# Optimization experiments

Measured on AMD Instinct MI355X. Metric: run time of the kernel, lower is better.

The kernel has to match this reference:

```python
import jax, jax.numpy as jnp
import numpy as np

DIM = 256
HEADS = 8
DK = DIM // HEADS
MLP_HID = 4 * DIM
EPS = 1e-5


def _ln(t, s, b):
    m = jnp.mean(t, axis=-1, keepdims=True)
    v = jnp.mean((t - m) ** 2, axis=-1, keepdims=True)
    return (t - m) / jnp.sqrt(v + EPS) * s + b


def setup_inputs() -> dict:
    key = jax.random.key(0)
    ks = jax.random.split(key, 32)
    B, N, C = 8, 128, DIM
    d = {}
    d["x"] = jax.random.normal(ks[0], (B, N, C), jnp.float32)
    d["y"] = jax.random.normal(ks[1], (B, N, N, C), jnp.float32)
    def lin(k, fi, fo):
        k1, k2 = jax.random.split(k)
        return (jax.random.normal(k1, (fi, fo), jnp.float32) * 0.02,
                jax.random.normal(k2, (fo,), jnp.float32) * 0.02)
    for i, nm in enumerate(["q", "k", "v", "e", "oe", "on"]):
        w, b = lin(ks[2 + i], C, C)
        d[f"W{nm}"], d[f"b{nm}"] = w, b
    for i, nm in enumerate(["mlp1", "mlp2"]):
        w1, b1 = lin(ks[10 + 2 * i], C, MLP_HID)
        w2, b2 = lin(ks[11 + 2 * i], MLP_HID, C)
        d[f"{nm}_w1"], d[f"{nm}_b1"] = w1, b1
        d[f"{nm}_w2"], d[f"{nm}_b2"] = w2, b2
    for i, nm in enumerate(["ln1", "ln3", "ln4", "ln5", "ln6"]):
        d[f"{nm}_s"] = jnp.ones((C,), jnp.float32)
        d[f"{nm}_b"] = jnp.zeros((C,), jnp.float32)
    return d


def reference(x, y, Wq, bq, Wk, bk, Wv, bv, We, be, Woe, boe, Won, bon,
              mlp1_w1, mlp1_b1, mlp1_w2, mlp1_b2,
              mlp2_w1, mlp2_b1, mlp2_w2, mlp2_b2,
              ln1_s, ln1_b, ln3_s, ln3_b, ln4_s, ln4_b,
              ln5_s, ln5_b, ln6_s, ln6_b):
    B, N, C = x.shape
    H, DKl = HEADS, DK

    x1 = _ln(x, ln1_s, ln1_b)

    # attention (elementwise q*k modulated by edge embeddings)
    q = (x1 @ Wq + bq).reshape(B, N, H, DKl)
    k = (x1 @ Wk + bk).reshape(B, N, H, DKl)
    v = (x1 @ Wv + bv).reshape(B, N, H, DKl)
    e = (y @ We + be).reshape(B, N, N, H, DKl)

    attn = q[:, :, None] * k[:, None, :]          # (B,N,N,H,DK)
    attn = attn / jnp.sqrt(jnp.float32(DKl))
    attn = attn * (e + 1.0) * e

    edge_out = attn.reshape(B, N, N, C) @ Woe + boe  # out_e
    p = jax.nn.softmax(attn, axis=2)                 # softmax over second n
    agg = jnp.einsum("bijhd,bjhd->bihd", p, v).reshape(B, N, C)
    node_out = agg @ Won + bon                       # out_n

    x2 = _ln(x1 + node_out, ln3_s, ln3_b)
    y2 = _ln(edge_out + y, ln4_s, ln4_b)

    mlp_x = jax.nn.relu(x2 @ mlp1_w1 + mlp1_b1) @ mlp1_w2 + mlp1_b2
    mlp_y = jax.nn.relu(y2 @ mlp2_w1 + mlp2_b1) @ mlp2_w2 + mlp2_b2

    x_out = _ln(x2 + mlp_x, ln5_s, ln5_b)
    y_out = _ln(y2 + mlp_y, ln6_s, ln6_b)
    return (x_out, y_out)
```

## Files before the change

kernel.cpp:

```cpp
#include <hip/hip_runtime.h>

#define CDIM 256
#define NSEQ 128
#define HID 1024
#define EPS 1e-5f
#define SCALE 0.17677669529663687f
#define ASTR 264
#define MROWS 64

typedef __attribute__((ext_vector_type(8))) short short8;
typedef __attribute__((ext_vector_type(4))) float f32x4;

static __device__ __forceinline__ unsigned short f2bf(float x) {
    unsigned u = __float_as_uint(x);
    u += 0x7fff + ((u >> 16) & 1);
    return (unsigned short)(u >> 16);
}
static __device__ __forceinline__ float bf2f(unsigned short h) {
    return __uint_as_float(((unsigned)h) << 16);
}

__global__ __launch_bounds__(256) void prep_w(const float* __restrict__ W,
        unsigned short* __restrict__ hi, unsigned short* __restrict__ lo,
        int N, int ksBits) {
    int idx = blockIdx.x * 256 + threadIdx.x;
    int j = idx & 7, lane = (idx >> 3) & 63, rest = idx >> 9;
    int ks = rest & ((1 << ksBits) - 1), nt = rest >> ksBits;
    int n = nt * 16 + (lane & 15);
    int kk = ks * 32 + ((lane >> 4) << 3) + j;
    float x = W[kk * N + n];
    unsigned short h = f2bf(x);
    hi[idx] = h;
    lo[idx] = f2bf(x - bf2f(h));
}

__device__ __forceinline__ float2 block_ln(float val, float* sred) {
    const int wave = threadIdx.x >> 6;
    const int lane = threadIdx.x & 63;
    float s = val, ss = val * val;
    #pragma unroll
    for (int off = 32; off; off >>= 1) {
        s  += __shfl_xor(s, off);
        ss += __shfl_xor(ss, off);
    }
    __syncthreads();
    if (lane == 0) { sred[wave] = s; sred[4 + wave] = ss; }
    __syncthreads();
    s  = sred[0] + sred[1] + sred[2] + sred[3];
    ss = sred[4] + sred[5] + sred[6] + sred[7];
    float mu = s * (1.f / 256.f);
    float rs = rsqrtf(ss * (1.f / 256.f) - mu * mu + EPS);
    return make_float2(mu, rs);
}

__global__ __launch_bounds__(256) void ln1_kernel(
    const float* __restrict__ x, const float* __restrict__ s,
    const float* __restrict__ b, float* __restrict__ x1) {
    __shared__ float sred[8];
    const int bi = blockIdx.x, t = threadIdx.x;
    float v = x[bi * CDIM + t];
    float2 mr = block_ln(v, sred);
    x1[bi * CDIM + t] = (v - mr.x) * mr.y * s[t] + b[t];
}

__global__ __launch_bounds__(256) void qkv_kernel(
    const float* __restrict__ x1,
    const float* __restrict__ Wq, const float* __restrict__ bq,
    const float* __restrict__ Wk, const float* __restrict__ bk,
    const float* __restrict__ Wv, const float* __restrict__ bv,
    float* __restrict__ q, float* __restrict__ k, float* __restrict__ v) {
    __shared__ float sX[CDIM];
    const int bi = blockIdx.x, t = threadIdx.x;
    sX[t] = x1[bi * CDIM + t];
    __syncthreads();
    float aq = bq[t], ak = bk[t], av = bv[t];
    for (int kk = 0; kk < CDIM; kk += 4) {
        float4 xv = *(const float4*)&sX[kk];
        #pragma unroll
        for (int d = 0; d < 4; ++d) {
            float xd = (d == 0) ? xv.x : (d == 1) ? xv.y : (d == 2) ? xv.z : xv.w;
            aq += xd * Wq[(kk + d) * CDIM + t];
            ak += xd * Wk[(kk + d) * CDIM + t];
            av += xd * Wv[(kk + d) * CDIM + t];
        }
    }
    q[bi * CDIM + t] = aq;
    k[bi * CDIM + t] = ak;
    v[bi * CDIM + t] = av;
}

static __device__ __forceinline__ void gemm16(
    const unsigned short* __restrict__ Ah, const unsigned short* __restrict__ Al,
    const unsigned short* __restrict__ Bh, const unsigned short* __restrict__ Bl,
    int nt0, int ksTotal, int ks0, int lane, f32x4 acc[4][2])
{
    const int l16 = lane & 15, quad = lane >> 4;
    #pragma unroll 2
    for (int ks = 0; ks < 8; ++ks) {
        short8 bh[2], bl[2];
        #pragma unroll
        for (int nt = 0; nt < 2; ++nt) {
            size_t off = ((size_t)((nt0 + nt) * ksTotal + (ks0 + ks)) * 64 + lane) * 8;
            bh[nt] = *(const short8*)(Bh + off);
            bl[nt] = *(const short8*)(Bl + off);
        }
        #pragma unroll
        for (int mt = 0; mt < 4; ++mt) {
            int ao = (mt * 16 + l16) * ASTR + ks * 32 + quad * 8;
            short8 ah = *(const short8*)(Ah + ao);
            short8 al = *(const short8*)(Al + ao);
            #pragma unroll
            for (int nt = 0; nt < 2; ++nt) {
                acc[mt][nt] = __builtin_amdgcn_mfma_f32_16x16x32_bf16(ah, bh[nt], acc[mt][nt], 0, 0, 0);
                acc[mt][nt] = __builtin_amdgcn_mfma_f32_16x16x32_bf16(ah, bl[nt], acc[mt][nt], 0, 0, 0);
                acc[mt][nt] = __builtin_amdgcn_mfma_f32_16x16x32_bf16(al, bh[nt], acc[mt][nt], 0, 0, 0);
            }
        }
    }
}

static __device__ __forceinline__ void ln_reduce(
    float pre[4][2][4], float* sSum, float* sSS, int w, int l16, int quad, int tid)
{
    #pragma unroll
    for (int mt = 0; mt < 4; ++mt)
        #pragma unroll
        for (int r = 0; r < 4; ++r) {
            float s  = pre[mt][0][r] + pre[mt][1][r];
            float ss = pre[mt][0][r] * pre[mt][0][r] + pre[mt][1][r] * pre[mt][1][r];
            #pragma unroll
            for (int off = 1; off < 16; off <<= 1) {
                s  += __shfl_xor(s, off);
                ss += __shfl_xor(ss, off);
            }
            if (l16 == 0) {
                int row = mt * 16 + quad * 4 + r;
                sSum[w * 64 + row] = s;
                sSS [w * 64 + row] = ss;
            }
        }
    __syncthreads();
    if (tid < 64) {
        float S = 0.f, SS2 = 0.f;
        #pragma unroll
        for (int ww = 0; ww < 8; ++ww) { S += sSum[ww * 64 + tid]; SS2 += sSS[ww * 64 + tid]; }
        float mu = S * (1.f / 256.f);
        float rs = rsqrtf(SS2 * (1.f / 256.f) - mu * mu + EPS);
        sSum[tid] = mu; sSS[tid] = rs;
    }
    __syncthreads();
}

__global__ __launch_bounds__(512, 2) void y_mega(
    const float* __restrict__ y, const float* __restrict__ qg, const float* __restrict__ kg,
    const unsigned short* __restrict__ WeH, const unsigned short* __restrict__ WeL,
    const float* __restrict__ be,
    const unsigned short* __restrict__ WoH, const unsigned short* __restrict__ WoL,
    const float* __restrict__ boe,
    const unsigned short* __restrict__ W1H, const unsigned short* __restrict__ W1L,
    const float* __restrict__ b1,
    const unsigned short* __restrict__ W2H, const unsigned short* __restrict__ W2L,
    const float* __restrict__ b2,
    const float* __restrict__ ln4s, const float* __restrict__ ln4b,
    const float* __restrict__ ln6s, const float* __restrict__ ln6b,
    unsigned short* __restrict__ attn_bf, float* __restrict__ yout)
{
    __shared__ unsigned short sAh[MROWS * ASTR], sAl[MROWS * ASTR];
    __shared__ unsigned short sHh[MROWS * ASTR], sHl[MROWS * ASTR];
    __shared__ float sSum[8 * 64], sSS[8 * 64];

    const int tid  = threadIdx.x;
    const int w    = tid >> 6, lane = tid & 63;
    const int l16  = lane & 15, quad = lane >> 4;
    const long long row0 = (long long)blockIdx.x * MROWS;
    const int b  = (int)(row0 >> 14);
    const int i  = (int)((row0 >> 7) & 127);
    const int j0 = (int)(row0 & 127);
    const float* qrow  = qg + ((b << 7) + i) * CDIM;
    const float* kbase = kg + ((b << 7) + j0) * CDIM;
    const int c0 = w * 32 + l16, c1 = c0 + 16;

    {
        int r  = tid >> 3;
        int cc = (tid & 7) * 32;
        const float* src = y + (row0 + r) * CDIM + cc;
        unsigned short hbuf[32], lbuf[32];
        #pragma unroll
        for (int e = 0; e < 32; e += 4) {
            float4 vv = *(const float4*)(src + e);
            float a[4] = {vv.x, vv.y, vv.z, vv.w};
            #pragma unroll
            for (int d = 0; d < 4; ++d) {
                unsigned short h = f2bf(a[d]);
                hbuf[e + d] = h;
                lbuf[e + d] = f2bf(a[d] - bf2f(h));
            }
        }
        #pragma unroll
        for (int e = 0; e < 32; e += 8) {
            *(short8*)&sAh[r * ASTR + cc + e] = *(short8*)&hbuf[e];
            *(short8*)&sAl[r * ASTR + cc + e] = *(short8*)&lbuf[e];
        }
    }
    __syncthreads();

    f32x4 acc[4][2];
    const f32x4 zf = {0.f, 0.f, 0.f, 0.f};

    #pragma unroll
    for (int mt = 0; mt < 4; ++mt) { acc[mt][0] = zf; acc[mt][1] = zf; }
    gemm16(sAh, sAl, WeH, WeL, w * 2, 8, 0, lane, acc);

    float q0 = qrow[c0], q1 = qrow[c1];
    float be0 = be[c0], be1 = be[c1];
    float attnv[4][2][4];
    #pragma unroll
    for (int mt = 0; mt < 4; ++mt)
        #pragma unroll
        for (int r = 0; r < 4; ++r) {
            int mloc = mt * 16 + quad * 4 + r;
            float k0 = kbase[mloc * CDIM + c0], k1 = kbase[mloc * CDIM + c1];
            float e0 = acc[mt][0][r] + be0, e1 = acc[mt][1][r] + be1;
            float a0 = q0 * k0 * SCALE * ((e0 + 1.f) * e0);
            float a1 = q1 * k1 * SCALE * ((e1 + 1.f) * e1);
            attnv[mt][0][r] = a0; attnv[mt][1][r] = a1;
            attn_bf[(row0 + mloc) * CDIM + c0] = f2bf(a0);
            attn_bf[(row0 + mloc) * CDIM + c1] = f2bf(a1);
        }
    __syncthreads();

    #pragma unroll
    for (int mt = 0; mt < 4; ++mt)
        #pragma unroll
        for (int r = 0; r < 4; ++r) {
            int mloc = mt * 16 + quad * 4 + r;
            #pragma unroll
            for (int nt = 0; nt < 2; ++nt) {
                int c = (nt == 0) ? c0 : c1;
                float a = attnv[mt][nt][r];
                unsigned short h = f2bf(a);
                sAh[mloc * ASTR + c] = h;
                sAl[mloc * ASTR + c] = f2bf(a - bf2f(h));
            }
        }
    __syncthreads();

    #pragma unroll
    for (int mt = 0; mt < 4; ++mt) { acc[mt][0] = zf; acc[mt][1] = zf; }
    gemm16(sAh, sAl, WoH, WoL, w * 2, 8, 0, lane, acc);

    float pre[4][2][4];
    float bo0 = boe[c0], bo1 = boe[c1];
    #pragma unroll
    for (int mt = 0; mt < 4; ++mt)
        #pragma unroll
        for (int r = 0; r < 4; ++r) {
            int mloc = mt * 16 + quad * 4 + r;
            pre[mt][0][r] = acc[mt][0][r] + bo0 + y[(row0 + mloc) * CDIM + c0];
            pre[mt][1][r] = acc[mt][1][r] + bo1 + y[(row0 + mloc) * CDIM + c1];
        }
    ln_reduce(pre, sSum, sSS, w, l16, quad, tid);

    float l4s0 = ln4s[c0], l4b0 = ln4b[c0], l4s1 = ln4s[c1], l4b1 = ln4b[c1];
    float y2v[4][2][4];
    #pragma unroll
    for (int mt = 0; mt < 4; ++mt)
        #pragma unroll
        for (int r = 0; r < 4; ++r) {
            int mloc = mt * 16 + quad * 4 + r;
            float mu = sSum[mloc], rs = sSS[mloc];
            float v0 = (pre[mt][0][r] - mu) * rs * l4s0 + l4b0;
            float v1 = (pre[mt][1][r] - mu) * rs * l4s1 + l4b1;
            y2v[mt][0][r] = v0; y2v[mt][1][r] = v1;
            unsigned short h0 = f2bf(v0), h1 = f2bf(v1);
            sAh[mloc * ASTR + c0] = h0; sAl[mloc * ASTR + c0] = f2bf(v0 - bf2f(h0));
            sAh[mloc * ASTR + c1] = h1; sAl[mloc * ASTR + c1] = f2bf(v1 - bf2f(h1));
        }
    __syncthreads();

    f32x4 out[4][2];
    #pragma unroll
    for (int mt = 0; mt < 4; ++mt) { out[mt][0] = zf; out[mt][1] = zf; }
    for (int qq = 0; qq < 4; ++qq) {
        f32x4 hh[4][2];
        #pragma unroll
        for (int mt = 0; mt < 4; ++mt) { hh[mt][0] = zf; hh[mt][1] = zf; }
        gemm16(sAh, sAl, W1H, W1L, qq * 16 + w * 2, 8, 0, lane, hh);
        float bb0 = b1[qq * 256 + c0], bb1 = b1[qq * 256 + c1];
        __syncthreads();
        #pragma unroll
        for (int mt = 0; mt < 4; ++mt)
            #pragma unroll
            for (int r = 0; r < 4; ++r) {
                int mloc = mt * 16 + quad * 4 + r;
                float h0 = fmaxf(hh[mt][0][r] + bb0, 0.f);
                float h1 = fmaxf(hh[mt][1][r] + bb1, 0.f);
                unsigned short hb0 = f2bf(h0), hb1 = f2bf(h1);
                sHh[mloc * ASTR + c0] = hb0; sHl[mloc * ASTR + c0] = f2bf(h0 - bf2f(hb0));
                sHh[mloc * ASTR + c1] = hb1; sHl[mloc * ASTR + c1] = f2bf(h1 - bf2f(hb1));
            }
        __syncthreads();
        gemm16(sHh, sHl, W2H, W2L, w * 2, 32, qq * 8, lane, out);
    }

    float b20 = b2[c0], b21 = b2[c1];
    #pragma unroll
    for (int mt = 0; mt < 4; ++mt)
        #pragma unroll
        for (int r = 0; r < 4; ++r) {
            pre[mt][0][r] = y2v[mt][0][r] + out[mt][0][r] + b20;
            pre[mt][1][r] = y2v[mt][1][r] + out[mt][1][r] + b21;
        }
    __syncthreads();
    ln_reduce(pre, sSum, sSS, w, l16, quad, tid);

    float l6s0 = ln6s[c0], l6b0 = ln6b[c0], l6s1 = ln6s[c1], l6b1 = ln6b[c1];
    #pragma unroll
    for (int mt = 0; mt < 4; ++mt)
        #pragma unroll
        for (int r = 0; r < 4; ++r) {
            int mloc = mt * 16 + quad * 4 + r;
            float mu = sSum[mloc], rs = sSS[mloc];
            yout[(row0 + mloc) * CDIM + c0] = (pre[mt][0][r] - mu) * rs * l6s0 + l6b0;
            yout[(row0 + mloc) * CDIM + c1] = (pre[mt][1][r] - mu) * rs * l6s1 + l6b1;
        }
}

__global__ __launch_bounds__(256) void softmax_agg(
    const unsigned short* __restrict__ attn, const float* __restrict__ v,
    float* __restrict__ agg) {
    const int bi = blockIdx.x, t = threadIdx.x;
    const unsigned short* ap = attn + (long long)bi * NSEQ * CDIM + t;
    const float* vp = v + (long long)(bi >> 7) * NSEQ * CDIM + t;
    float m = -1e30f;
    for (int j = 0; j < NSEQ; ++j) m = fmaxf(m, bf2f(ap[j * CDIM]));
    float s = 0.f, o = 0.f;
    for (int j = 0; j < NSEQ; ++j) {
        float ex = __expf(bf2f(ap[j * CDIM]) - m);
        s += ex;
        o += ex * vp[j * CDIM];
    }
    agg[bi * CDIM + t] = o / s;
}

__global__ __launch_bounds__(256) void x_path(
    const float* __restrict__ x1, const float* __restrict__ agg,
    const float* __restrict__ Won, const float* __restrict__ bon,
    const float* __restrict__ ln3s, const float* __restrict__ ln3b,
    const float* __restrict__ w1, const float* __restrict__ b1,
    const float* __restrict__ w2, const float* __restrict__ b2,
    const float* __restrict__ ln5s, const float* __restrict__ ln5b,
    float* __restrict__ xout) {
    __shared__ float sG[CDIM];
    __shared__ float sX2[CDIM];
    __shared__ float sH[HID];
    __shared__ float sred[8];
    const int bi = blockIdx.x, t = threadIdx.x;
    sG[t] = agg[bi * CDIM + t];
    __syncthreads();
    float no = bon[t];
    for (int kk = 0; kk < CDIM; kk += 4) {
        float4 gv = *(const float4*)&sG[kk];
        no += gv.x * Won[(kk + 0) * CDIM + t] + gv.y * Won[(kk + 1) * CDIM + t]
            + gv.z * Won[(kk + 2) * CDIM + t] + gv.w * Won[(kk + 3) * CDIM + t];
    }
    float pre = x1[bi * CDIM + t] + no;
    float2 mr = block_ln(pre, sred);
    float x2 = (pre - mr.x) * mr.y * ln3s[t] + ln3b[t];
    sX2[t] = x2;
    __syncthreads();
    float h[4];
    #pragma unroll
    for (int m = 0; m < 4; ++m) h[m] = b1[t + 256 * m];
    for (int kk = 0; kk < CDIM; kk += 4) {
        float4 xv = *(const float4*)&sX2[kk];
        #pragma unroll
        for (int m = 0; m < 4; ++m) {
            int u = t + 256 * m;
            h[m] += xv.x * w1[(kk + 0) * HID + u] + xv.y * w1[(kk + 1) * HID + u]
                  + xv.z * w1[(kk + 2) * HID + u] + xv.w * w1[(kk + 3) * HID + u];
        }
    }
    #pragma unroll
    for (int m = 0; m < 4; ++m) sH[t + 256 * m] = fmaxf(h[m], 0.f);
    __syncthreads();
    float o = b2[t];
    for (int u = 0; u < HID; u += 4) {
        float4 hv = *(const float4*)&sH[u];
        o += hv.x * w2[(u + 0) * CDIM + t] + hv.y * w2[(u + 1) * CDIM + t]
           + hv.z * w2[(u + 2) * CDIM + t] + hv.w * w2[(u + 3) * CDIM + t];
    }
    float pre2 = x2 + o;
    float2 mr2 = block_ln(pre2, sred);
    xout[bi * CDIM + t] = (pre2 - mr2.x) * mr2.y * ln5s[t] + ln5b[t];
}

extern "C" void kernel_launch(void* const* d_in, const int* in_sizes, int n_in,
                              void* d_out, int out_size, void* d_ws, size_t ws_size,
                              hipStream_t stream) {
    const float* x   = (const float*)d_in[0];
    const float* y   = (const float*)d_in[1];
    const float* Wq  = (const float*)d_in[2];  const float* bq  = (const float*)d_in[3];
    const float* Wk  = (const float*)d_in[4];  const float* bk  = (const float*)d_in[5];
    const float* Wv  = (const float*)d_in[6];  const float* bv  = (const float*)d_in[7];
    const float* We  = (const float*)d_in[8];  const float* be  = (const float*)d_in[9];
    const float* Woe = (const float*)d_in[10]; const float* boe = (const float*)d_in[11];
    const float* Won = (const float*)d_in[12]; const float* bon = (const float*)d_in[13];
    const float* m1w1= (const float*)d_in[14]; const float* m1b1= (const float*)d_in[15];
    const float* m1w2= (const float*)d_in[16]; const float* m1b2= (const float*)d_in[17];
    const float* m2w1= (const float*)d_in[18]; const float* m2b1= (const float*)d_in[19];
    const float* m2w2= (const float*)d_in[20]; const float* m2b2= (const float*)d_in[21];
    const float* ln1s= (const float*)d_in[22]; const float* ln1b= (const float*)d_in[23];
    const float* ln3s= (const float*)d_in[24]; const float* ln3b= (const float*)d_in[25];
    const float* ln4s= (const float*)d_in[26]; const float* ln4b= (const float*)d_in[27];
    const float* ln5s= (const float*)d_in[28]; const float* ln5b= (const float*)d_in[29];
    const float* ln6s= (const float*)d_in[30]; const float* ln6b= (const float*)d_in[31];

    const int BN  = 8 * 128;
    const long long BNN = 8LL * 128 * 128;

    float* ws  = (float*)d_ws;
    float* x1  = ws;
    float* q   = x1 + BN * CDIM;
    float* k   = q  + BN * CDIM;
    float* v   = k  + BN * CDIM;
    float* agg = v  + BN * CDIM;
    unsigned short* attn_bf = (unsigned short*)(agg + BN * CDIM);
    unsigned short* WeH = attn_bf + BNN * CDIM;
    unsigned short* WeL = WeH + 65536;
    unsigned short* WoH = WeL + 65536;
    unsigned short* WoL = WoH + 65536;
    unsigned short* W1H = WoL + 65536;
    unsigned short* W1L = W1H + 262144;
    unsigned short* W2H = W1L + 262144;
    unsigned short* W2L = W2H + 262144;

    float* xout = (float*)d_out;
    float* yout = xout + BN * CDIM;

    prep_w<<<256,  256, 0, stream>>>(We,   WeH, WeL, 256,  3);
    prep_w<<<256,  256, 0, stream>>>(Woe,  WoH, WoL, 256,  3);
    prep_w<<<1024, 256, 0, stream>>>(m2w1, W1H, W1L, 1024, 3);
    prep_w<<<1024, 256, 0, stream>>>(m2w2, W2H, W2L, 256,  5);

    ln1_kernel<<<BN, 256, 0, stream>>>(x, ln1s, ln1b, x1);
    qkv_kernel<<<BN, 256, 0, stream>>>(x1, Wq, bq, Wk, bk, Wv, bv, q, k, v);

    y_mega<<<(int)(BNN / MROWS), 512, 0, stream>>>(
        y, q, k, WeH, WeL, be, WoH, WoL, boe,
        W1H, W1L, m2b1, W2H, W2L, m2b2,
        ln4s, ln4b, ln6s, ln6b, attn_bf, yout);

    softmax_agg<<<BN, 256, 0, stream>>>(attn_bf, v, agg);
    x_path<<<BN, 256, 0, stream>>>(x1, agg, Won, bon, ln3s, ln3b,
                                   m1w1, m1b1, m1w2, m1b2, ln5s, ln5b, xout);
}
```

Measured before the change: 991.9 us.

## Shrink edge tile, drop low-bf16 weight terms, fuse prep and LN/QKV, batch node rows

The edge mega-kernel tile drops from 64 to 32 rows and the occupancy hint rises to 4 blocks per CU. The Woe, MLP1 and MLP2 GEMMs now use a two-term split-bf16 product instead of three, which skips the weight low-part MFMA and its loads at some cost in accuracy. The four weight-prep launches merge into one, and LN1 and QKV fuse into a single kernel that handles 4 rows per block. Softmax-aggregate splits j across two thread teams with paired-channel loads, and x_path processes 4 rows per block to reuse weight loads.

```diff
diff --git a/kernel.cpp b/kernel.cpp
--- a/kernel.cpp
+++ b/kernel.cpp
@@ -6,7 +6,7 @@
 #define EPS 1e-5f
 #define SCALE 0.17677669529663687f
 #define ASTR 264
-#define MROWS 64
+#define MROWS 32
 
 typedef __attribute__((ext_vector_type(8))) short short8;
 typedef __attribute__((ext_vector_type(4))) float f32x4;
@@ -20,79 +20,91 @@
     return __uint_as_float(((unsigned)h) << 16);
 }
 
-__global__ __launch_bounds__(256) void prep_w(const float* __restrict__ W,
-        unsigned short* __restrict__ hi, unsigned short* __restrict__ lo,
-        int N, int ksBits) {
-    int idx = blockIdx.x * 256 + threadIdx.x;
+__global__ __launch_bounds__(256) void prep_all(
+    const float* __restrict__ We, const float* __restrict__ Woe,
+    const float* __restrict__ W1, const float* __restrict__ W2,
+    unsigned short* __restrict__ WeH, unsigned short* __restrict__ WeL,
+    unsigned short* __restrict__ WoH, unsigned short* __restrict__ W1H,
+    unsigned short* __restrict__ W2H) {
+    int blk = blockIdx.x;
+    const float* W; unsigned short* H; unsigned short* L = nullptr;
+    int N, ksBits, base;
+    if (blk < 256)       { W = We;  H = WeH; L = WeL; N = 256;  ksBits = 3; base = 0; }
+    else if (blk < 512)  { W = Woe; H = WoH; N = 256;  ksBits = 3; base = 256; }
+    else if (blk < 1536) { W = W1;  H = W1H; N = 1024; ksBits = 3; base = 512; }
+    else                 { W = W2;  H = W2H; N = 256;  ksBits = 5; base = 1536; }
+    int idx = (blk - base) * 256 + threadIdx.x;
     int j = idx & 7, lane = (idx >> 3) & 63, rest = idx >> 9;
     int ks = rest & ((1 << ksBits) - 1), nt = rest >> ksBits;
-    int n = nt * 16 + (lane & 15);
+    int n  = nt * 16 + (lane & 15);
     int kk = ks * 32 + ((lane >> 4) << 3) + j;
     float x = W[kk * N + n];
     unsigned short h = f2bf(x);
-    hi[idx] = h;
-    lo[idx] = f2bf(x - bf2f(h));
-}
-
-__device__ __forceinline__ float2 block_ln(float val, float* sred) {
-    const int wave = threadIdx.x >> 6;
-    const int lane = threadIdx.x & 63;
-    float s = val, ss = val * val;
-    #pragma unroll
-    for (int off = 32; off; off >>= 1) {
-        s  += __shfl_xor(s, off);
-        ss += __shfl_xor(ss, off);
-    }
-    __syncthreads();
-    if (lane == 0) { sred[wave] = s; sred[4 + wave] = ss; }
-    __syncthreads();
-    s  = sred[0] + sred[1] + sred[2] + sred[3];
-    ss = sred[4] + sred[5] + sred[6] + sred[7];
-    float mu = s * (1.f / 256.f);
-    float rs = rsqrtf(ss * (1.f / 256.f) - mu * mu + EPS);
-    return make_float2(mu, rs);
-}
-
-__global__ __launch_bounds__(256) void ln1_kernel(
-    const float* __restrict__ x, const float* __restrict__ s,
-    const float* __restrict__ b, float* __restrict__ x1) {
-    __shared__ float sred[8];
-    const int bi = blockIdx.x, t = threadIdx.x;
-    float v = x[bi * CDIM + t];
-    float2 mr = block_ln(v, sred);
-    x1[bi * CDIM + t] = (v - mr.x) * mr.y * s[t] + b[t];
-}
-
-__global__ __launch_bounds__(256) void qkv_kernel(
-    const float* __restrict__ x1,
+    H[idx] = h;
+    if (L) L[idx] = f2bf(x - bf2f(h));
+}
+
+__global__ __launch_bounds__(256) void lnqkv_kernel(
+    const float* __restrict__ x,
+    const float* __restrict__ ln1s, const float* __restrict__ ln1b,
     const float* __restrict__ Wq, const float* __restrict__ bq,
     const float* __restrict__ Wk, const float* __restrict__ bk,
     const float* __restrict__ Wv, const float* __restrict__ bv,
+    float* __restrict__ x1,
     float* __restrict__ q, float* __restrict__ k, float* __restrict__ v) {
-    __shared__ float sX[CDIM];
-    const int bi = blockIdx.x, t = threadIdx.x;
-    sX[t] = x1[bi * CDIM + t];
-    __syncthreads();
-    float aq = bq[t], ak = bk[t], av = bv[t];
-    for (int kk = 0; kk < CDIM; kk += 4) {
-        float4 xv = *(const float4*)&sX[kk];
-        #pragma unroll
-        for (int d = 0; d < 4; ++d) {
-            float xd = (d == 0) ? xv.x : (d == 1) ? xv.y : (d == 2) ? xv.z : xv.w;
-            aq += xd * Wq[(kk + d) * CDIM + t];
-            ak += xd * Wk[(kk + d) * CDIM + t];
-            av += xd * Wv[(kk + d) * CDIM + t];
-        }
-    }
-    q[bi * CDIM + t] = aq;
-    k[bi * CDIM + t] = ak;
-    v[bi * CDIM + t] = av;
-}
-
-static __device__ __forceinline__ void gemm16(
-    const unsigned short* __restrict__ Ah, const unsigned short* __restrict__ Al,
+    __shared__ float sX[4][CDIM];
+    __shared__ float sMu[4], sRs[4];
+    const int bi0 = blockIdx.x * 4, t = threadIdx.x;
+    const int w = t >> 6, lane = t & 63;
+    float xv[4];
+    #pragma unroll
+    for (int r = 0; r < 4; ++r) { xv[r] = x[(bi0 + r) * CDIM + t]; sX[r][t] = xv[r]; }
+    __syncthreads();
+    {
+        float s = 0.f, ss = 0.f;
+        #pragma unroll
+        for (int m = 0; m < 4; ++m) { float a = sX[w][lane + 64 * m]; s += a; ss += a * a; }
+        #pragma unroll
+        for (int off = 32; off; off >>= 1) { s += __shfl_xor(s, off); ss += __shfl_xor(ss, off); }
+        if (lane == 0) {
+            float mu = s * (1.f / 256.f);
+            sMu[w] = mu;
+            sRs[w] = rsqrtf(ss * (1.f / 256.f) - mu * mu + EPS);
+        }
+    }
+    __syncthreads();
+    #pragma unroll
+    for (int r = 0; r < 4; ++r) {
+        float xn = (xv[r] - sMu[r]) * sRs[r] * ln1s[t] + ln1b[t];
+        sX[r][t] = xn;
+        x1[(bi0 + r) * CDIM + t] = xn;
+    }
+    __syncthreads();
+    float aq[4], ak[4], av[4];
+    #pragma unroll
+    for (int r = 0; r < 4; ++r) { aq[r] = bq[t]; ak[r] = bk[t]; av[r] = bv[t]; }
+    #pragma unroll 4
+    for (int kk = 0; kk < CDIM; ++kk) {
+        float wq = Wq[kk * CDIM + t], wk = Wk[kk * CDIM + t], wv = Wv[kk * CDIM + t];
+        #pragma unroll
+        for (int r = 0; r < 4; ++r) {
+            float xd = sX[r][kk];
+            aq[r] += xd * wq; ak[r] += xd * wk; av[r] += xd * wv;
+        }
+    }
+    #pragma unroll
+    for (int r = 0; r < 4; ++r) {
+        q[(bi0 + r) * CDIM + t] = aq[r];
+        k[(bi0 + r) * CDIM + t] = ak[r];
+        v[(bi0 + r) * CDIM + t] = av[r];
+    }
+}
+
+template <int TERMS>
+static __device__ __forceinline__ void gemmN(
+    const unsigned short* Ah, const unsigned short* Al,
     const unsigned short* __restrict__ Bh, const unsigned short* __restrict__ Bl,
-    int nt0, int ksTotal, int ks0, int lane, f32x4 acc[4][2])
+    int nt0, int ksTotal, int ks0, int lane, f32x4 acc[2][2])
 {
     const int l16 = lane & 15, quad = lane >> 4;
     #pragma unroll 2
@@ -102,28 +114,29 @@
         for (int nt = 0; nt < 2; ++nt) {
             size_t off = ((size_t)((nt0 + nt) * ksTotal + (ks0 + ks)) * 64 + lane) * 8;
             bh[nt] = *(const short8*)(Bh + off);
-            bl[nt] = *(const short8*)(Bl + off);
-        }
-        #pragma unroll
-        for (int mt = 0; mt < 4; ++mt) {
+            if (TERMS == 3) bl[nt] = *(const short8*)(Bl + off);
+        }
+        #pragma unroll
+        for (int mt = 0; mt < 2; ++mt) {
             int ao = (mt * 16 + l16) * ASTR + ks * 32 + quad * 8;
             short8 ah = *(const short8*)(Ah + ao);
             short8 al = *(const short8*)(Al + ao);
             #pragma unroll
             for (int nt = 0; nt < 2; ++nt) {
                 acc[mt][nt] = __builtin_amdgcn_mfma_f32_16x16x32_bf16(ah, bh[nt], acc[mt][nt], 0, 0, 0);
-                acc[mt][nt] = __builtin_amdgcn_mfma_f32_16x16x32_bf16(ah, bl[nt], acc[mt][nt], 0, 0, 0);
                 acc[mt][nt] = __builtin_amdgcn_mfma_f32_16x16x32_bf16(al, bh[nt], acc[mt][nt], 0, 0, 0);
+                if (TERMS == 3)
+                    acc[mt][nt] = __builtin_amdgcn_mfma_f32_16x16x32_bf16(ah, bl[nt], acc[mt][nt], 0, 0, 0);
             }
         }
     }
 }
 
-static __device__ __forceinline__ void ln_reduce(
-    float pre[4][2][4], float* sSum, float* sSS, int w, int l16, int quad, int tid)
+static __device__ __forceinline__ void ln_reduce32(
+    float pre[2][2][4], float* sSum, float* sSS, int w, int l16, int quad, int tid)
 {
     #pragma unroll
-    for (int mt = 0; mt < 4; ++mt)
+    for (int mt = 0; mt < 2; ++mt)
         #pragma unroll
         for (int r = 0; r < 4; ++r) {
             float s  = pre[mt][0][r] + pre[mt][1][r];
@@ -135,15 +148,15 @@
             }
             if (l16 == 0) {
                 int row = mt * 16 + quad * 4 + r;
-                sSum[w * 64 + row] = s;
-                sSS [w * 64 + row] = ss;
+                sSum[w * 32 + row] = s;
+                sSS [w * 32 + row] = ss;
             }
         }
     __syncthreads();
-    if (tid < 64) {
+    if (tid < 32) {
         float S = 0.f, SS2 = 0.f;
         #pragma unroll
-        for (int ww = 0; ww < 8; ++ww) { S += sSum[ww * 64 + tid]; SS2 += sSS[ww * 64 + tid]; }
+        for (int ww = 0; ww < 8; ++ww) { S += sSum[ww * 32 + tid]; SS2 += sSS[ww * 32 + tid]; }
         float mu = S * (1.f / 256.f);
         float rs = rsqrtf(SS2 * (1.f / 256.f) - mu * mu + EPS);
         sSum[tid] = mu; sSS[tid] = rs;
@@ -151,23 +164,20 @@
     __syncthreads();
 }
 
-__global__ __launch_bounds__(512, 2) void y_mega(
+__global__ __launch_bounds__(512, 4) void y_mega(
     const float* __restrict__ y, const float* __restrict__ qg, const float* __restrict__ kg,
     const unsigned short* __restrict__ WeH, const unsigned short* __restrict__ WeL,
     const float* __restrict__ be,
-    const unsigned short* __restrict__ WoH, const unsigned short* __restrict__ WoL,
-    const float* __restrict__ boe,
-    const unsigned short* __restrict__ W1H, const unsigned short* __restrict__ W1L,
-    const float* __restrict__ b1,
-    const unsigned short* __restrict__ W2H, const unsigned short* __restrict__ W2L,
-    const float* __restrict__ b2,
+    const unsigned short* __restrict__ WoH, const float* __restrict__ boe,
+    const unsigned short* __restrict__ W1H, const float* __restrict__ b1,
+    const unsigned short* __restrict__ W2H, const float* __restrict__ b2,
     const float* __restrict__ ln4s, const float* __restrict__ ln4b,
     const float* __restrict__ ln6s, const float* __restrict__ ln6b,
     unsigned short* __restrict__ attn_bf, float* __restrict__ yout)
 {
     __shared__ unsigned short sAh[MROWS * ASTR], sAl[MROWS * ASTR];
     __shared__ unsigned short sHh[MROWS * ASTR], sHl[MROWS * ASTR];
-    __shared__ float sSum[8 * 64], sSS[8 * 64];
+    __shared__ float sSum[8 * 32], sSS[8 * 32];
 
     const int tid  = threadIdx.x;
     const int w    = tid >> 6, lane = tid & 63;
@@ -181,12 +191,12 @@
     const int c0 = w * 32 + l16, c1 = c0 + 16;
 
     {
-        int r  = tid >> 3;
-        int cc = (tid & 7) * 32;
+        int r  = tid >> 4;
+        int cc = (tid & 15) * 16;
         const float* src = y + (row0 + r) * CDIM + cc;
-        unsigned short hbuf[32], lbuf[32];
-        #pragma unroll
-        for (int e = 0; e < 32; e += 4) {
+        unsigned short hbuf[16], lbuf[16];
+        #pragma unroll
+        for (int e = 0; e < 16; e += 4) {
             float4 vv = *(const float4*)(src + e);
             float a[4] = {vv.x, vv.y, vv.z, vv.w};
             #pragma unroll
@@ -197,25 +207,25 @@
             }
         }
         #pragma unroll
-        for (int e = 0; e < 32; e += 8) {
+        for (int e = 0; e < 16; e += 8) {
             *(short8*)&sAh[r * ASTR + cc + e] = *(short8*)&hbuf[e];
             *(short8*)&sAl[r * ASTR + cc + e] = *(short8*)&lbuf[e];
         }
     }
     __syncthreads();
 
-    f32x4 acc[4][2];
+    f32x4 acc[2][2];
     const f32x4 zf = {0.f, 0.f, 0.f, 0.f};
 
     #pragma unroll
-    for (int mt = 0; mt < 4; ++mt) { acc[mt][0] = zf; acc[mt][1] = zf; }
-    gemm16(sAh, sAl, WeH, WeL, w * 2, 8, 0, lane, acc);
+    for (int mt = 0; mt < 2; ++mt) { acc[mt][0] = zf; acc[mt][1] = zf; }
+    gemmN<3>(sAh, sAl, WeH, WeL, w * 2, 8, 0, lane, acc);
 
     float q0 = qrow[c0], q1 = qrow[c1];
     float be0 = be[c0], be1 = be[c1];
-    float attnv[4][2][4];
-    #pragma unroll
-    for (int mt = 0; mt < 4; ++mt)
+    float attnv[2][2][4];
+    #pragma unroll
+    for (int mt = 0; mt < 2; ++mt)
         #pragma unroll
         for (int r = 0; r < 4; ++r) {
             int mloc = mt * 16 + quad * 4 + r;
@@ -230,7 +240,7 @@
     __syncthreads();
 
     #pragma unroll
-    for (int mt = 0; mt < 4; ++mt)
+    for (int mt = 0; mt < 2; ++mt)
         #pragma unroll
         for (int r = 0; r < 4; ++r) {
             int mloc = mt * 16 + quad * 4 + r;
@@ -246,25 +256,25 @@
     __syncthreads();
 
     #pragma unroll
-    for (int mt = 0; mt < 4; ++mt) { acc[mt][0] = zf; acc[mt][1] = zf; }
-    gemm16(sAh, sAl, WoH, WoL, w * 2, 8, 0, lane, acc);
-
-    float pre[4][2][4];
+    for (int mt = 0; mt < 2; ++mt) { acc[mt][0] = zf; acc[mt][1] = zf; }
+    gemmN<2>(sAh, sAl, WoH, nullptr, w * 2, 8, 0, lane, acc);
+
+    float pre[2][2][4];
     float bo0 = boe[c0], bo1 = boe[c1];
     #pragma unroll
-    for (int mt = 0; mt < 4; ++mt)
+    for (int mt = 0; mt < 2; ++mt)
         #pragma unroll
         for (int r = 0; r < 4; ++r) {
             int mloc = mt * 16 + quad * 4 + r;
             pre[mt][0][r] = acc[mt][0][r] + bo0 + y[(row0 + mloc) * CDIM + c0];
             pre[mt][1][r] = acc[mt][1][r] + bo1 + y[(row0 + mloc) * CDIM + c1];
         }
-    ln_reduce(pre, sSum, sSS, w, l16, quad, tid);
+    ln_reduce32(pre, sSum, sSS, w, l16, quad, tid);
 
     float l4s0 = ln4s[c0], l4b0 = ln4b[c0], l4s1 = ln4s[c1], l4b1 = ln4b[c1];
-    float y2v[4][2][4];
-    #pragma unroll
-    for (int mt = 0; mt < 4; ++mt)
+    float y2v[2][2][4];
+    #pragma unroll
+    for (int mt = 0; mt < 2; ++mt)
         #pragma unroll
         for (int r = 0; r < 4; ++r) {
             int mloc = mt * 16 + quad * 4 + r;
@@ -278,18 +288,18 @@
         }
     __syncthreads();
 
-    f32x4 out[4][2];
-    #pragma unroll
-    for (int mt = 0; mt < 4; ++mt) { out[mt][0] = zf; out[mt][1] = zf; }
+    f32x4 out[2][2];
+    #pragma unroll
+    for (int mt = 0; mt < 2; ++mt) { out[mt][0] = zf; out[mt][1] = zf; }
     for (int qq = 0; qq < 4; ++qq) {
-        f32x4 hh[4][2];
-        #pragma unroll
-        for (int mt = 0; mt < 4; ++mt) { hh[mt][0] = zf; hh[mt][1] = zf; }
-        gemm16(sAh, sAl, W1H, W1L, qq * 16 + w * 2, 8, 0, lane, hh);
+        f32x4 hh[2][2];
+        #pragma unroll
+        for (int mt = 0; mt < 2; ++mt) { hh[mt][0] = zf; hh[mt][1] = zf; }
+        gemmN<2>(sAh, sAl, W1H, nullptr, qq * 16 + w * 2, 8, 0, lane, hh);
         float bb0 = b1[qq * 256 + c0], bb1 = b1[qq * 256 + c1];
         __syncthreads();
         #pragma unroll
-        for (int mt = 0; mt < 4; ++mt)
+        for (int mt = 0; mt < 2; ++mt)
             #pragma unroll
             for (int r = 0; r < 4; ++r) {
                 int mloc = mt * 16 + quad * 4 + r;
@@ -300,23 +310,22 @@
                 sHh[mloc * ASTR + c1] = hb1; sHl[mloc * ASTR + c1] = f2bf(h1 - bf2f(hb1));
             }
         __syncthreads();
-        gemm16(sHh, sHl, W2H, W2L, w * 2, 32, qq * 8, lane, out);
+        gemmN<2>(sHh, sHl, W2H, nullptr, w * 2, 32, qq * 8, lane, out);
     }
 
     float b20 = b2[c0], b21 = b2[c1];
     #pragma unroll
-    for (int mt = 0; mt < 4; ++mt)
+    for (int mt = 0; mt < 2; ++mt)
         #pragma unroll
         for (int r = 0; r < 4; ++r) {
             pre[mt][0][r] = y2v[mt][0][r] + out[mt][0][r] + b20;
             pre[mt][1][r] = y2v[mt][1][r] + out[mt][1][r] + b21;
         }
-    __syncthreads();
-    ln_reduce(pre, sSum, sSS, w, l16, quad, tid);
+    ln_reduce32(pre, sSum, sSS, w, l16, quad, tid);
 
     float l6s0 = ln6s[c0], l6b0 = ln6b[c0], l6s1 = ln6s[c1], l6b1 = ln6b[c1];
     #pragma unroll
-    for (int mt = 0; mt < 4; ++mt)
+    for (int mt = 0; mt < 2; ++mt)
         #pragma unroll
         for (int r = 0; r < 4; ++r) {
             int mloc = mt * 16 + quad * 4 + r;
@@ -329,18 +338,42 @@
 __global__ __launch_bounds__(256) void softmax_agg(
     const unsigned short* __restrict__ attn, const float* __restrict__ v,
     float* __restrict__ agg) {
+    __shared__ float2 sM[2][128], sS[2][128], sO[2][128];
     const int bi = blockIdx.x, t = threadIdx.x;
-    const unsigned short* ap = attn + (long long)bi * NSEQ * CDIM + t;
-    const float* vp = v + (long long)(bi >> 7) * NSEQ * CDIM + t;
-    float m = -1e30f;
-    for (int j = 0; j < NSEQ; ++j) m = fmaxf(m, bf2f(ap[j * CDIM]));
-    float s = 0.f, o = 0.f;
-    for (int j = 0; j < NSEQ; ++j) {
-        float ex = __expf(bf2f(ap[j * CDIM]) - m);
-        s += ex;
-        o += ex * vp[j * CDIM];
-    }
-    agg[bi * CDIM + t] = o / s;
+    const int c2 = t & 127, team = t >> 7, ch = c2 * 2;
+    const unsigned short* ap = attn + (size_t)bi * NSEQ * CDIM + ch;
+    const float* vp = v + (size_t)(bi >> 7) * NSEQ * CDIM + ch;
+    const int jb = team * 64;
+    float m0 = -1e30f, m1 = -1e30f;
+    #pragma unroll 4
+    for (int j = jb; j < jb + 64; ++j) {
+        unsigned uu = *(const unsigned*)(ap + (size_t)j * CDIM);
+        m0 = fmaxf(m0, bf2f((unsigned short)uu));
+        m1 = fmaxf(m1, bf2f((unsigned short)(uu >> 16)));
+    }
+    sM[team][c2] = make_float2(m0, m1);
+    __syncthreads();
+    float2 mo = sM[team ^ 1][c2];
+    m0 = fmaxf(m0, mo.x); m1 = fmaxf(m1, mo.y);
+    float s0 = 0.f, s1 = 0.f, o0 = 0.f, o1 = 0.f;
+    #pragma unroll 4
+    for (int j = jb; j < jb + 64; ++j) {
+        unsigned uu = *(const unsigned*)(ap + (size_t)j * CDIM);
+        float e0 = __expf(bf2f((unsigned short)uu) - m0);
+        float e1 = __expf(bf2f((unsigned short)(uu >> 16)) - m1);
+        float2 vv = *(const float2*)(vp + (size_t)j * CDIM);
+        s0 += e0; s1 += e1;
+        o0 += e0 * vv.x; o1 += e1 * vv.y;
+    }
+    sS[team][c2] = make_float2(s0, s1);
+    sO[team][c2] = make_float2(o0, o1);
+    __syncthreads();
+    if (team == 0) {
+        float2 s2 = sS[1][c2], o2 = sO[1][c2];
+        float r0 = (o0 + o2.x) / (s0 + s2.x);
+        float r1 = (o1 + o2.y) / (s1 + s2.y);
+        *(float2*)(agg + (size_t)bi * CDIM + ch) = make_float2(r0, r1);
+    }
 }
 
 __global__ __launch_bounds__(256) void x_path(
@@ -351,48 +384,102 @@
     const float* __restrict__ w2, const float* __restrict__ b2,
     const float* __restrict__ ln5s, const float* __restrict__ ln5b,
     float* __restrict__ xout) {
-    __shared__ float sG[CDIM];
-    __shared__ float sX2[CDIM];
-    __shared__ float sH[HID];
-    __shared__ float sred[8];
-    const int bi = blockIdx.x, t = threadIdx.x;
-    sG[t] = agg[bi * CDIM + t];
-    __syncthreads();
-    float no = bon[t];
-    for (int kk = 0; kk < CDIM; kk += 4) {
-        float4 gv = *(const float4*)&sG[kk];
-        no += gv.x * Won[(kk + 0) * CDIM + t] + gv.y * Won[(kk + 1) * CDIM + t]
-            + gv.z * Won[(kk + 2) * CDIM + t] + gv.w * Won[(kk + 3) * CDIM + t];
-    }
-    float pre = x1[bi * CDIM + t] + no;
-    float2 mr = block_ln(pre, sred);
-    float x2 = (pre - mr.x) * mr.y * ln3s[t] + ln3b[t];
-    sX2[t] = x2;
-    __syncthreads();
-    float h[4];
-    #pragma unroll
-    for (int m = 0; m < 4; ++m) h[m] = b1[t + 256 * m];
-    for (int kk = 0; kk < CDIM; kk += 4) {
-        float4 xv = *(const float4*)&sX2[kk];
-        #pragma unroll
-        for (int m = 0; m < 4; ++m) {
-            int u = t + 256 * m;
-            h[m] += xv.x * w1[(kk + 0) * HID + u] + xv.y * w1[(kk + 1) * HID + u]
-                  + xv.z * w1[(kk + 2) * HID + u] + xv.w * w1[(kk + 3) * HID + u];
-        }
-    }
-    #pragma unroll
-    for (int m = 0; m < 4; ++m) sH[t + 256 * m] = fmaxf(h[m], 0.f);
-    __syncthreads();
-    float o = b2[t];
-    for (int u = 0; u < HID; u += 4) {
-        float4 hv = *(const float4*)&sH[u];
-        o += hv.x * w2[(u + 0) * CDIM + t] + hv.y * w2[(u + 1) * CDIM + t]
-           + hv.z * w2[(u + 2) * CDIM + t] + hv.w * w2[(u + 3) * CDIM + t];
-    }
-    float pre2 = x2 + o;
-    float2 mr2 = block_ln(pre2, sred);
-    xout[bi * CDIM + t] = (pre2 - mr2.x) * mr2.y * ln5s[t] + ln5b[t];
+    __shared__ float sG[4][CDIM];
+    __shared__ float sP[4][CDIM];
+    __shared__ float sH[4][HID];
+    __shared__ float sMu[4], sRs[4];
+    const int bi0 = blockIdx.x * 4, t = threadIdx.x;
+    const int w = t >> 6, lane = t & 63;
+    #pragma unroll
+    for (int r = 0; r < 4; ++r) sG[r][t] = agg[(bi0 + r) * CDIM + t];
+    __syncthreads();
+    float no[4];
+    #pragma unroll
+    for (int r = 0; r < 4; ++r) no[r] = bon[t];
+    #pragma unroll 4
+    for (int kk = 0; kk < CDIM; ++kk) {
+        float wv = Won[kk * CDIM + t];
+        #pragma unroll
+        for (int r = 0; r < 4; ++r) no[r] += sG[r][kk] * wv;
+    }
+    float pre[4];
+    #pragma unroll
+    for (int r = 0; r < 4; ++r) {
+        pre[r] = x1[(bi0 + r) * CDIM + t] + no[r];
+        sP[r][t] = pre[r];
+    }
+    __syncthreads();
+    {
+        float s = 0.f, ss = 0.f;
+        #pragma unroll
+        for (int m = 0; m < 4; ++m) { float a = sP[w][lane + 64 * m]; s += a; ss += a * a; }
+        #pragma unroll
+        for (int off = 32; off; off >>= 1) { s += __shfl_xor(s, off); ss += __shfl_xor(ss, off); }
+        if (lane == 0) {
+            float mu = s * (1.f / 256.f);
+            sMu[w] = mu; sRs[w] = rsqrtf(ss * (1.f / 256.f) - mu * mu + EPS);
+        }
+    }
+    __syncthreads();
+    float x2[4];
+    #pragma unroll
+    for (int r = 0; r < 4; ++r) {
+        x2[r] = (pre[r] - sMu[r]) * sRs[r] * ln3s[t] + ln3b[t];
+        sP[r][t] = x2[r];
+    }
+    __syncthreads();
+    float h[4][4];
+    #pragma unroll
+    for (int m = 0; m < 4; ++m) {
+        float bb = b1[t + 256 * m];
+        #pragma unroll
+        for (int r = 0; r < 4; ++r) h[r][m] = bb;
+    }
+    #pragma unroll 2
+    for (int kk = 0; kk < CDIM; ++kk) {
+        float wv[4];
+        #pragma unroll
+        for (int m = 0; m < 4; ++m) wv[m] = w1[kk * HID + t + 256 * m];
+        #pragma unroll
+        for (int r = 0; r < 4; ++r) {
+            float xd = sP[r][kk];
+            #pragma unroll
+            for (int m = 0; m < 4; ++m) h[r][m] += xd * wv[m];
+        }
+    }
+    #pragma unroll
+    for (int r = 0; r < 4; ++r)
+        #pragma unroll
+        for (int m = 0; m < 4; ++m) sH[r][t + 256 * m] = fmaxf(h[r][m], 0.f);
+    __syncthreads();
+    float o[4];
+    #pragma unroll
+    for (int r = 0; r < 4; ++r) o[r] = b2[t];
+    #pragma unroll 4
+    for (int u = 0; u < HID; ++u) {
+        float wv = w2[u * CDIM + t];
+        #pragma unroll
+        for (int r = 0; r < 4; ++r) o[r] += sH[r][u] * wv;
+    }
+    float pre2[4];
+    #pragma unroll
+    for (int r = 0; r < 4; ++r) { pre2[r] = x2[r] + o[r]; sP[r][t] = pre2[r]; }
+    __syncthreads();
+    {
+        float s = 0.f, ss = 0.f;
+        #pragma unroll
+        for (int m = 0; m < 4; ++m) { float a = sP[w][lane + 64 * m]; s += a; ss += a * a; }
+        #pragma unroll
+        for (int off = 32; off; off >>= 1) { s += __shfl_xor(s, off); ss += __shfl_xor(ss, off); }
+        if (lane == 0) {
+            float mu = s * (1.f / 256.f);
+            sMu[w] = mu; sRs[w] = rsqrtf(ss * (1.f / 256.f) - mu * mu + EPS);
+        }
+    }
+    __syncthreads();
+    #pragma unroll
+    for (int r = 0; r < 4; ++r)
+        xout[(bi0 + r) * CDIM + t] = (pre2[r] - sMu[r]) * sRs[r] * ln5s[t] + ln5b[t];
 }
 
 extern "C" void kernel_launch(void* const* d_in, const int* in_sizes, int n_in,
@@ -429,29 +516,19 @@
     unsigned short* WeH = attn_bf + BNN * CDIM;
     unsigned short* WeL = WeH + 65536;
     unsigned short* WoH = WeL + 65536;
-    unsigned short* WoL = WoH + 65536;
-    unsigned short* W1H = WoL + 65536;
-    unsigned short* W1L = W1H + 262144;
-    unsigned short* W2H = W1L + 262144;
-    unsigned short* W2L = W2H + 262144;
+    unsigned short* W1H = WoH + 65536;
+    unsigned short* W2H = W1H + 262144;
 
     float* xout = (float*)d_out;
     float* yout = xout + BN * CDIM;
 
-    prep_w<<<256,  256, 0, stream>>>(We,   WeH, WeL, 256,  3);
-    prep_w<<<256,  256, 0, stream>>>(Woe,  WoH, WoL, 256,  3);
-    prep_w<<<1024, 256, 0, stream>>>(m2w1, W1H, W1L, 1024, 3);
-    prep_w<<<1024, 256, 0, stream>>>(m2w2, W2H, W2L, 256,  5);
-
-    ln1_kernel<<<BN, 256, 0, stream>>>(x, ln1s, ln1b, x1);
-    qkv_kernel<<<BN, 256, 0, stream>>>(x1, Wq, bq, Wk, bk, Wv, bv, q, k, v);
-
+    prep_all<<<2560, 256, 0, stream>>>(We, Woe, m2w1, m2w2, WeH, WeL, WoH, W1H, W2H);
+    lnqkv_kernel<<<BN / 4, 256, 0, stream>>>(x, ln1s, ln1b, Wq, bq, Wk, bk, Wv, bv,
+                                             x1, q, k, v);
     y_mega<<<(int)(BNN / MROWS), 512, 0, stream>>>(
-        y, q, k, WeH, WeL, be, WoH, WoL, boe,
-        W1H, W1L, m2b1, W2H, W2L, m2b2,
+        y, q, k, WeH, WeL, be, WoH, boe, W1H, m2b1, W2H, m2b2,
         ln4s, ln4b, ln6s, ln6b, attn_bf, yout);
-
     softmax_agg<<<BN, 256, 0, stream>>>(attn_bf, v, agg);
-    x_path<<<BN, 256, 0, stream>>>(x1, agg, Won, bon, ln3s, ln3b,
-                                   m1w1, m1b1, m1w2, m1b2, ln5s, ln5b, xout);
-}
+    x_path<<<BN / 4, 256, 0, stream>>>(x1, agg, Won, bon, ln3s, ln3b,
+                                       m1w1, m1b1, m1w2, m1b2, ln5s, ln5b, xout);
+}
```

After: 872.7 us. 1.14x faster.
